# Optimization experiments

Measured on AMD Instinct MI355X. Metric: run time of the kernel, lower is better.

Reference implementation:

```python
import jax, jax.numpy as jnp
import numpy as np
from jax import lax

B, N, C = 16, 2304, 768
H_HEADS, D = 12, 64  # num_heads, head_dim
SCALE = 9.0 ** (-0.5)  # equivalent_head_dim ** -0.5


def setup_inputs() -> dict:
    key = jax.random.key(0)
    ks = jax.random.split(key, 8)
    return {
        "x": jax.random.normal(ks[0], (B, N, C), dtype=jnp.float32),
        "qkv_w": jax.random.normal(ks[1], (3 * C + 3 * D, C), dtype=jnp.float32) * 0.02,
        "qkv_b": jax.random.normal(ks[2], (3 * C + 3 * D,), dtype=jnp.float32) * 0.02,
        "w1": jax.random.normal(ks[3], (1, H_HEADS, D, D), dtype=jnp.float32) * 0.02,
        "w2": jax.random.normal(ks[4], (1, H_HEADS, D, D), dtype=jnp.float32) * 0.02,
        "w3": jax.random.normal(ks[5], (D, 1, 3, 3), dtype=jnp.float32) * 0.02,
        "proj_w": jax.random.normal(ks[6], (C, C + D), dtype=jnp.float32) * 0.02,
        "proj_b": jax.random.normal(ks[7], (C,), dtype=jnp.float32) * 0.02,
        "h": 48,
        "w": 48,
    }


def _inner_swiglu(k, v, w1, w2, lr=1.0):
    # k, v: [B, H, N, d]; w1, w2: [1, H, d, d]
    z1 = jnp.einsum('bhnd,hde->bhne', k, w1[0])
    z2 = jnp.einsum('bhnd,hde->bhne', k, w2[0])
    sig = jax.nn.sigmoid(z2)
    a = z2 * sig
    e = -v / float(v.shape[2]) * SCALE
    g1 = jnp.einsum('bhnd,bhne->bhde', k, e * a)
    g2 = jnp.einsum('bhnd,bhne->bhde', k, e * z1 * (sig * (1.0 + z2 * (1.0 - sig))))
    g1 = g1 / (jnp.linalg.norm(g1, axis=-2, keepdims=True) + 1.0)
    g2 = g2 / (jnp.linalg.norm(g2, axis=-2, keepdims=True) + 1.0)
    return w1 - lr * g1, w2 - lr * g2  # [B, H, d, d]


def _inner_3x3dwc(k, v, w3, hh, ww, lr=1.0):
    # k, v: [B, d, h, w]; w3: [d, 1, 3, 3]
    b, c = k.shape[0], k.shape[1]
    e = -v / float(hh * ww) * SCALE
    kp = jnp.pad(k, ((0, 0), (0, 0), (1, 1), (1, 1)))
    dots = []
    for ys in (0, 1, 2):  # 1 + dy
        for xs in (0, 1, 2):  # 1 + dx
            dots.append(jnp.sum(kp[:, :, ys:ys + hh, xs:xs + ww] * e, axis=(-2, -1)))
    g = jnp.stack(dots, axis=-1).reshape(b * c, 1, 3, 3)
    g = g / (jnp.sqrt(jnp.sum(g * g, axis=(-2, -1), keepdims=True)) + 1.0)
    return jnp.tile(w3, (b, 1, 1, 1)) - lr * g  # [B*d, 1, 3, 3]


def reference(x, qkv_w, qkv_b, w1, w2, w3, proj_w, proj_b, h, w):
    b, n, c = x.shape
    nh = w1.shape[1]
    d = c // nh
    qkv = x @ qkv_w.T + qkv_b  # [B, N, 3C + 3d]
    q1, k1, v1, q2, k2, v2 = jnp.split(
        qkv, [c, 2 * c, 3 * c, 3 * c + d, 3 * c + 2 * d], axis=-1)
    heads = lambda t: t.reshape(b, n, nh, d).transpose(0, 2, 1, 3)
    q1, k1, v1 = heads(q1), heads(k1), heads(v1)

    w1u, w2u = _inner_swiglu(k1, v1, w1, w2)
    x1 = jnp.einsum('bhnd,bhde->bhne', q1, w1u) * jax.nn.silu(
        jnp.einsum('bhnd,bhde->bhne', q1, w2u))
    x1 = x1.transpose(0, 2, 1, 3).reshape(b, n, c)

    spatial = lambda t: t.reshape(b, h, w, d).transpose(0, 3, 1, 2)  # [B, d, h, w]
    q2s, k2s, v2s = spatial(q2), spatial(k2), spatial(v2)
    w3u = _inner_3x3dwc(k2s, v2s, w3, h, w)
    x2 = lax.conv_general_dilated(
        q2s.reshape(1, b * d, h, w), w3u,
        window_strides=(1, 1), padding=((1, 1), (1, 1)),
        feature_group_count=b * d,
        dimension_numbers=('NCHW', 'OIHW', 'NCHW'))
    x2 = x2.reshape(b, d, n).transpose(0, 2, 1)  # [B, N, d]

    out = jnp.concatenate([x1, x2], axis=-1) @ proj_w.T + proj_b
    return out
```

## Files before the change

kernel.cpp:

```cpp
#include <hip/hip_runtime.h>
#include <hip/hip_bf16.h>
#include <math.h>

#define B_   16
#define N_   2304
#define C_   768
#define H_   12
#define D_   64
#define M_   (B_*N_)
#define NQKV 2496
#define NPAD 2560
#define CCP  896
#define EVS  (-1.0f/6912.0f)

typedef __bf16 bf16x8 __attribute__((ext_vector_type(8)));
typedef __bf16 bf16x4 __attribute__((ext_vector_type(4)));
typedef float  f32x4  __attribute__((ext_vector_type(4)));

static __device__ __forceinline__ void gload_lds16(const void* g, void* l) {
  __builtin_amdgcn_global_load_lds((const __attribute__((address_space(1))) void*)g,
                                   (__attribute__((address_space(3))) void*)l, 16, 0, 0);
}

static __device__ __forceinline__ bf16x8 ld8(const __bf16* p) {
  bf16x4 lo = *(const bf16x4*)p;
  bf16x4 hi = *(const bf16x4*)(p + 4);
  return __builtin_shufflevector(lo, hi, 0,1,2,3,4,5,6,7);
}

__global__ __launch_bounds__(256) void cvt_x(const float* __restrict__ in,
                                             __bf16* __restrict__ out, int n8) {
  int i = blockIdx.x * 256 + threadIdx.x;
  if (i >= n8) return;
  const float4* p = (const float4*)(in + (size_t)i * 8);
  float4 a = p[0], b = p[1];
  bf16x8 o = {(__bf16)a.x,(__bf16)a.y,(__bf16)a.z,(__bf16)a.w,
              (__bf16)b.x,(__bf16)b.y,(__bf16)b.z,(__bf16)b.w};
  *(bf16x8*)(out + (size_t)i * 8) = o;
}

__global__ __launch_bounds__(256) void cvt_wqkv(const float* __restrict__ w,
    const float* __restrict__ bias, __bf16* __restrict__ wout, float* __restrict__ bout) {
  int i = blockIdx.x * 256 + threadIdx.x;
  if (i < NPAD * 96) {
    int n = i / 96, c8 = i - n * 96;
    bf16x8 o;
    if (n < NQKV) {
      const float4* p = (const float4*)(w + (size_t)n * 768 + c8 * 8);
      float4 a = p[0], b = p[1];
      o = (bf16x8){(__bf16)a.x,(__bf16)a.y,(__bf16)a.z,(__bf16)a.w,
                   (__bf16)b.x,(__bf16)b.y,(__bf16)b.z,(__bf16)b.w};
    } else {
      o = (bf16x8){(__bf16)0.f,(__bf16)0.f,(__bf16)0.f,(__bf16)0.f,
                   (__bf16)0.f,(__bf16)0.f,(__bf16)0.f,(__bf16)0.f};
    }
    *(bf16x8*)(wout + (size_t)n * 768 + c8 * 8) = o;
  }
  if (i < NPAD) bout[i] = (i < NQKV) ? bias[i] : 0.0f;
}

__global__ __launch_bounds__(256) void cvt_pw(const float* __restrict__ in,
                                              __bf16* __restrict__ out) {
  int i = blockIdx.x * 256 + threadIdx.x;
  if (i >= 86016) return;
  int n = i / 112, c8 = i - n * 112;
  int k = c8 * 8;
  bf16x8 o;
  if (k < 832) {
    const float4* p = (const float4*)(in + (size_t)n * 832 + k);
    float4 a = p[0], b = p[1];
    o = (bf16x8){(__bf16)a.x,(__bf16)a.y,(__bf16)a.z,(__bf16)a.w,
                 (__bf16)b.x,(__bf16)b.y,(__bf16)b.z,(__bf16)b.w};
  } else {
    o = (bf16x8){(__bf16)0.f,(__bf16)0.f,(__bf16)0.f,(__bf16)0.f,
                 (__bf16)0.f,(__bf16)0.f,(__bf16)0.f,(__bf16)0.f};
  }
  *(bf16x8*)(out + (size_t)n * CCP + k) = o;
}

__global__ __launch_bounds__(256) void zeropad(__bf16* __restrict__ concat) {
  int i = blockIdx.x * 256 + threadIdx.x;
  if (i >= M_ * 8) return;
  int row = i >> 3, ch = i & 7;
  bf16x8 z = {(__bf16)0.f,(__bf16)0.f,(__bf16)0.f,(__bf16)0.f,
              (__bf16)0.f,(__bf16)0.f,(__bf16)0.f,(__bf16)0.f};
  *(bf16x8*)(concat + (size_t)row * CCP + 832 + ch * 8) = z;
}

template<int OUTF32>
__global__ __launch_bounds__(512, 2) void gemm8(
    const __bf16* __restrict__ A, const __bf16* __restrict__ Bt,
    const float* __restrict__ bias, void* __restrict__ Cout,
    const int K, const int ldc, const int nbn, const int KT)
{
  __shared__ __align__(16) __bf16 sA[2][2][128 * 64];
  __shared__ __align__(16) __bf16 sB[2][2][128 * 64];
  const int tid  = threadIdx.x;
  const int lane = tid & 63;
  const int wid  = tid >> 6;
  const int wm = wid >> 2;
  const int wn = wid & 3;
  const int l15 = lane & 15, lq = lane >> 4;

  const int nwg = gridDim.x;
  const int swz = ((int)blockIdx.x & 7) * (nwg >> 3) + ((int)blockIdx.x >> 3);
  const int bm = swz / nbn;
  const int bn = swz - bm * nbn;

  const int strow = tid >> 3;
  const int stoff = strow * 64 + (tid & 7) * 8;
  const __bf16* gA = A  + (size_t)((size_t)bm * 256 + strow) * K + ((tid & 7) ^ (strow & 7)) * 8;
  const __bf16* gB = Bt + (size_t)((size_t)bn * 256 + strow) * K + ((tid & 7) ^ (strow & 7)) * 8;

  f32x4 acc[2][4][2][2];
  #pragma unroll
  for (int a = 0; a < 2; ++a)
    #pragma unroll
    for (int m = 0; m < 4; ++m)
      #pragma unroll
      for (int b = 0; b < 2; ++b)
        #pragma unroll
        for (int n = 0; n < 2; ++n) acc[a][m][b][n] = (f32x4){0.f,0.f,0.f,0.f};

  bf16x8 af0[4][2], af1[4][2], bf0[2][2], bf1[2][2];

#define STAGE_A(q, h, T) do {                                                   \
    const size_t ko_ = (size_t)(T) * 64;                                        \
    gload_lds16(gA + (size_t)((h)*128 +  0) * K + ko_, &sA[q][h][stoff]);       \
    gload_lds16(gA + (size_t)((h)*128 + 64) * K + ko_, &sA[q][h][4096 + stoff]);\
  } while (0)
#define STAGE_B(q, h, T) do {                                                   \
    const size_t ko_ = (size_t)(T) * 64;                                        \
    gload_lds16(gB + (size_t)((h)*128 +  0) * K + ko_, &sB[q][h][stoff]);       \
    gload_lds16(gB + (size_t)((h)*128 + 64) * K + ko_, &sB[q][h][4096 + stoff]);\
  } while (0)
#define LOADA(DST, h, q) do {                                                   \
    _Pragma("unroll") for (int mf_ = 0; mf_ < 4; ++mf_) {                       \
      const int r_ = wm * 64 + mf_ * 16 + l15;                                  \
      _Pragma("unroll") for (int kk_ = 0; kk_ < 2; ++kk_)                       \
        DST[mf_][kk_] = *(const bf16x8*)&sA[q][h][r_ * 64 + (((kk_*4+lq) ^ (r_&7)) * 8)]; \
    } } while (0)
#define LOADB(DST, h, q) do {                                                   \
    _Pragma("unroll") for (int nf_ = 0; nf_ < 2; ++nf_) {                       \
      const int c_ = wn * 32 + nf_ * 16 + l15;                                  \
      _Pragma("unroll") for (int kk_ = 0; kk_ < 2; ++kk_)                       \
        DST[nf_][kk_] = *(const bf16x8*)&sB[q][h][c_ * 64 + (((kk_*4+lq) ^ (c_&7)) * 8)]; \
    } } while (0)
#define MMA(a_, b_, AF, BF) do {                                                \
    __builtin_amdgcn_s_setprio(1);                                              \
    _Pragma("unroll") for (int kk_ = 0; kk_ < 2; ++kk_)                         \
    _Pragma("unroll") for (int mf_ = 0; mf_ < 4; ++mf_)                         \
    _Pragma("unroll") for (int nf_ = 0; nf_ < 2; ++nf_)                         \
      acc[a_][mf_][b_][nf_] = __builtin_amdgcn_mfma_f32_16x16x32_bf16(          \
          AF[mf_][kk_], BF[nf_][kk_], acc[a_][mf_][b_][nf_], 0, 0, 0);          \
    __builtin_amdgcn_s_setprio(0);                                              \
  } while (0)
#define BAR  __builtin_amdgcn_s_barrier()
#define LGKM do { asm volatile("s_waitcnt lgkmcnt(0)" ::: "memory");            \
                  __builtin_amdgcn_sched_barrier(0); } while (0)
#define VMW4 asm volatile("s_waitcnt vmcnt(4)" ::: "memory")
#define VMW0 asm volatile("s_waitcnt vmcnt(0)" ::: "memory")

  STAGE_A(0, 0, 0); STAGE_A(0, 1, 0); STAGE_B(0, 0, 0); STAGE_B(0, 1, 0);
  STAGE_B(1, 0, 1);
  STAGE_A(1, 1, 1);
  VMW4;
  BAR;

  for (int t = 0; t < KT; t += 2) {
    LOADA(af0, 0, 0); LOADB(bf0, 0, 0);
    STAGE_A(1, 0, t + 1); STAGE_B(1, 1, t + 1);
    BAR; LGKM; MMA(0, 0, af0, bf0); BAR;
    LOADA(af1, 1, 0);
    BAR; LGKM; MMA(1, 0, af1, bf0); BAR;
    LOADB(bf1, 1, 0);
    if (t + 2 < KT) STAGE_B(0, 0, t + 2);
    BAR; LGKM; MMA(1, 1, af1, bf1); BAR;
    if (t + 2 < KT) STAGE_A(0, 1, t + 2);
    BAR; MMA(0, 1, af0, bf1);
    if (t + 2 < KT) { VMW4; } else { VMW0; }
    BAR;
    LOADA(af0, 0, 1); LOADB(bf0, 0, 1);
    if (t + 2 < KT) { STAGE_A(0, 0, t + 2); STAGE_B(0, 1, t + 2); }
    BAR; LGKM; MMA(0, 0, af0, bf0); BAR;
    LOADA(af1, 1, 1);
    BAR; LGKM; MMA(1, 0, af1, bf0); BAR;
    LOADB(bf1, 1, 1);
    if (t + 3 < KT) STAGE_B(1, 0, t + 3);
    BAR; LGKM; MMA(1, 1, af1, bf1); BAR;
    if (t + 3 < KT) STAGE_A(1, 1, t + 3);
    BAR; MMA(0, 1, af0, bf1);
    if (t + 3 < KT) { VMW4; } else { VMW0; }
    BAR;
  }
#undef STAGE_A
#undef STAGE_B
#undef LOADA
#undef LOADB
#undef MMA

  #pragma unroll
  for (int b = 0; b < 2; ++b)
    #pragma unroll
    for (int nf = 0; nf < 2; ++nf) {
      const int col = bn * 256 + b * 128 + wn * 32 + nf * 16 + l15;
      const float bs = bias[col];
      #pragma unroll
      for (int a = 0; a < 2; ++a)
        #pragma unroll
        for (int mf = 0; mf < 4; ++mf) {
          const int row0 = bm * 256 + a * 128 + wm * 64 + mf * 16 + lq * 4;
          #pragma unroll
          for (int r = 0; r < 4; ++r) {
            float v = acc[a][mf][b][nf][r] + bs;
            if (OUTF32) ((float*)Cout)[(size_t)(row0 + r) * ldc + col] = v;
            else        ((__bf16*)Cout)[(size_t)(row0 + r) * ldc + col] = (__bf16)v;
          }
        }
    }
}

__global__ __launch_bounds__(256, 3) void inner_grad(
    const __bf16* __restrict__ qkv, const float* __restrict__ w1,
    const float* __restrict__ w2, float* __restrict__ gpart)
{
  const int blk = blockIdx.x;
  const int bh = blk >> 2, seg = blk & 3;
  const int b = bh / H_, h = bh - b * H_;
  const int tid = threadIdx.x, wid = tid >> 6, lane = tid & 63;
  const int wr = wid >> 1, wc = wid & 1, l15 = lane & 15, lq = lane >> 4;

  __shared__ __bf16 w1T[64 * 72], w2T[64 * 72];
  __shared__ __bf16 kNt1[64 * 72];
  __shared__ __bf16 kT[64 * 72], t2T[64 * 72];

  const float* w1p = w1 + h * 4096;
  const float* w2p = w2 + h * 4096;
  for (int idx = tid; idx < 4096; idx += 256) {
    int d = idx >> 6, e = idx & 63;
    w1T[e * 72 + d] = (__bf16)w1p[idx];
    w2T[e * 72 + d] = (__bf16)w2p[idx];
  }

  f32x4 g1a[2][2], g2a[2][2];
  #pragma unroll
  for (int i = 0; i < 2; ++i)
    #pragma unroll
    for (int j = 0; j < 2; ++j) { g1a[i][j] = (f32x4){0.f,0.f,0.f,0.f}; g2a[i][j] = (f32x4){0.f,0.f,0.f,0.f}; }

  const size_t rowb = (size_t)b * N_;
  const int koff = C_ + h * D_;
  const int voff = 2 * C_ + h * D_;
  const int sn = tid >> 2, sdb = tid & 3;
  __syncthreads();

  for (int ci = 0; ci < 9; ++ci) {
    const int n0 = seg * 576 + ci * 64;
    {
      const __bf16* src = qkv + (rowb + n0 + sn) * (size_t)NPAD + koff + sdb * 16;
      bf16x8 va = *(const bf16x8*)src;
      bf16x8 vb = *(const bf16x8*)(src + 8);
      __bf16* kn = &kNt1[sn * 72 + sdb * 16];
      *(bf16x4*)(kn + 0)  = __builtin_shufflevector(va, va, 0,1,2,3);
      *(bf16x4*)(kn + 4)  = __builtin_shufflevector(va, va, 4,5,6,7);
      *(bf16x4*)(kn + 8)  = __builtin_shufflevector(vb, vb, 0,1,2,3);
      *(bf16x4*)(kn + 12) = __builtin_shufflevector(vb, vb, 4,5,6,7);
      #pragma unroll
      for (int j = 0; j < 8; ++j) kT[(sdb * 16 + j) * 72 + sn] = va[j];
      #pragma unroll
      for (int j = 0; j < 8; ++j) kT[(sdb * 16 + 8 + j) * 72 + sn] = vb[j];
    }
    __syncthreads();

    f32x4 z1[2][2], z2[2][2];
    #pragma unroll
    for (int i = 0; i < 2; ++i)
      #pragma unroll
      for (int j = 0; j < 2; ++j) { z1[i][j] = (f32x4){0.f,0.f,0.f,0.f}; z2[i][j] = (f32x4){0.f,0.f,0.f,0.f}; }
    #pragma unroll
    for (int kk = 0; kk < 2; ++kk) {
      bf16x8 af[2], b1[2], b2[2];
      #pragma unroll
      for (int mi = 0; mi < 2; ++mi)
        af[mi] = ld8(&kNt1[(wr * 32 + mi * 16 + l15) * 72 + kk * 32 + lq * 8]);
      #pragma unroll
      for (int ni = 0; ni < 2; ++ni) {
        int e = wc * 32 + ni * 16 + l15;
        b1[ni] = ld8(&w1T[e * 72 + kk * 32 + lq * 8]);
        b2[ni] = ld8(&w2T[e * 72 + kk * 32 + lq * 8]);
      }
      #pragma unroll
      for (int mi = 0; mi < 2; ++mi)
        #pragma unroll
        for (int ni = 0; ni < 2; ++ni) {
          z1[mi][ni] = __builtin_amdgcn_mfma_f32_16x16x32_bf16(af[mi], b1[ni], z1[mi][ni], 0, 0, 0);
          z2[mi][ni] = __builtin_amdgcn_mfma_f32_16x16x32_bf16(af[mi], b2[ni], z2[mi][ni], 0, 0, 0);
        }
    }
    __syncthreads();

    #pragma unroll
    for (int mi = 0; mi < 2; ++mi)
      #pragma unroll
      for (int ni = 0; ni < 2; ++ni) {
        int nl = wr * 32 + mi * 16 + lq * 4;
        int e  = wc * 32 + ni * 16 + l15;
        const __bf16* vp = qkv + (rowb + n0 + nl) * (size_t)NPAD + voff + e;
        #pragma unroll
        for (int r = 0; r < 4; ++r) {
          float vv  = (float)vp[(size_t)r * NPAD];
          float ev  = vv * EVS;
          float z1v = z1[mi][ni][r], z2v = z2[mi][ni][r];
          float sg  = 1.0f / (1.0f + __expf(-z2v));
          float t1  = ev * (z2v * sg);
          float t2  = ev * z1v * (sg * (1.0f + z2v * (1.0f - sg)));
          kNt1[e * 72 + nl + r] = (__bf16)t1;
          t2T [e * 72 + nl + r] = (__bf16)t2;
        }
      }
    __syncthreads();

    #pragma unroll
    for (int kk = 0; kk < 2; ++kk) {
      bf16x8 af[2], b1[2], b2[2];
      #pragma unroll
      for (int mi = 0; mi < 2; ++mi)
        af[mi] = ld8(&kT[(wr * 32 + mi * 16 + l15) * 72 + kk * 32 + lq * 8]);
      #pragma unroll
      for (int ni = 0; ni < 2; ++ni) {
        int e = wc * 32 + ni * 16 + l15;
        b1[ni] = ld8(&kNt1[e * 72 + kk * 32 + lq * 8]);
        b2[ni] = ld8(&t2T [e * 72 + kk * 32 + lq * 8]);
      }
      #pragma unroll
      for (int mi = 0; mi < 2; ++mi)
        #pragma unroll
        for (int ni = 0; ni < 2; ++ni) {
          g1a[mi][ni] = __builtin_amdgcn_mfma_f32_16x16x32_bf16(af[mi], b1[ni], g1a[mi][ni], 0, 0, 0);
          g2a[mi][ni] = __builtin_amdgcn_mfma_f32_16x16x32_bf16(af[mi], b2[ni], g2a[mi][ni], 0, 0, 0);
        }
    }
    __syncthreads();
  }

  float* gp = gpart + (size_t)blk * 8192;
  #pragma unroll
  for (int mi = 0; mi < 2; ++mi)
    #pragma unroll
    for (int ni = 0; ni < 2; ++ni)
      #pragma unroll
      for (int r = 0; r < 4; ++r) {
        int d = wr * 32 + mi * 16 + lq * 4 + r;
        int e = wc * 32 + ni * 16 + l15;
        gp[d * 64 + e]        = g1a[mi][ni][r];
        gp[4096 + d * 64 + e] = g2a[mi][ni][r];
      }
}

__global__ __launch_bounds__(256) void inner_upd(
    const float* __restrict__ gpart, const float* __restrict__ w1,
    const float* __restrict__ w2, __bf16* __restrict__ wu)
{
  const int bh = blockIdx.x;
  const int h = bh % H_;
  const int tid = threadIdx.x;
  __shared__ float g1[64 * 65], g2[64 * 65];
  __shared__ float nrm1[64], nrm2[64];
  const float* w1p = w1 + h * 4096;
  const float* w2p = w2 + h * 4096;

  for (int idx = tid; idx < 4096; idx += 256) {
    float s1 = 0.f, s2 = 0.f;
    #pragma unroll
    for (int s = 0; s < 4; ++s) {
      const float* gp = gpart + (size_t)(bh * 4 + s) * 8192;
      s1 += gp[idx]; s2 += gp[4096 + idx];
    }
    int d = idx >> 6, e = idx & 63;
    g1[d * 65 + e] = s1; g2[d * 65 + e] = s2;
  }
  __syncthreads();
  if (tid < 128) {
    const float* gs = (tid < 64) ? g1 : g2;
    int e = tid & 63;
    float s = 0.f;
    for (int d = 0; d < 64; ++d) { float gv = gs[d * 65 + e]; s += gv * gv; }
    float rn = 1.0f / (sqrtf(s) + 1.0f);
    if (tid < 64) nrm1[e] = rn; else nrm2[e] = rn;
  }
  __syncthreads();
  __bf16* wub = wu + (size_t)bh * 8192;
  for (int idx = tid; idx < 4096; idx += 256) {
    int d = idx >> 6, e = idx & 63;
    wub[idx]        = (__bf16)(w1p[idx] - g1[d * 65 + e] * nrm1[e]);
    wub[4096 + idx] = (__bf16)(w2p[idx] - g2[d * 65 + e] * nrm2[e]);
  }
}

__global__ __launch_bounds__(256) void inner_apply(
    const __bf16* __restrict__ qkv, const __bf16* __restrict__ wu,
    __bf16* __restrict__ concat)
{
  const int blk = blockIdx.x;
  const int bh = blk / 6, seg = blk - bh * 6;
  const int b = bh / H_, h = bh - b * H_;
  const int tid = threadIdx.x, wid = tid >> 6, lane = tid & 63;
  const int wr = wid >> 1, wc = wid & 1, l15 = lane & 15, lq = lane >> 4;

  __shared__ __bf16 w1T[64 * 72], w2T[64 * 72], qN[64 * 72];
  const __bf16* wub = wu + (size_t)bh * 8192;
  for (int idx = tid; idx < 4096; idx += 256) {
    int d = idx >> 6, e = idx & 63;
    w1T[e * 72 + d] = wub[idx];
    w2T[e * 72 + d] = wub[4096 + idx];
  }

  const size_t rowb = (size_t)b * N_;
  const int qoff = h * D_;
  const int sn = tid >> 2, sdb = tid & 3;

  for (int ci = 0; ci < 6; ++ci) {
    const int n0 = seg * 384 + ci * 64;
    {
      const __bf16* src = qkv + (rowb + n0 + sn) * (size_t)NPAD + qoff + sdb * 16;
      bf16x8 va = *(const bf16x8*)src;
      bf16x8 vb = *(const bf16x8*)(src + 8);
      __bf16* kn = &qN[sn * 72 + sdb * 16];
      *(bf16x4*)(kn + 0)  = __builtin_shufflevector(va, va, 0,1,2,3);
      *(bf16x4*)(kn + 4)  = __builtin_shufflevector(va, va, 4,5,6,7);
      *(bf16x4*)(kn + 8)  = __builtin_shufflevector(vb, vb, 0,1,2,3);
      *(bf16x4*)(kn + 12) = __builtin_shufflevector(vb, vb, 4,5,6,7);
    }
    __syncthreads();
    f32x4 y1[2][2], y2[2][2];
    #pragma unroll
    for (int i = 0; i < 2; ++i)
      #pragma unroll
      for (int j = 0; j < 2; ++j) { y1[i][j] = (f32x4){0.f,0.f,0.f,0.f}; y2[i][j] = (f32x4){0.f,0.f,0.f,0.f}; }
    #pragma unroll
    for (int kk = 0; kk < 2; ++kk) {
      bf16x8 af[2], b1[2], b2[2];
      #pragma unroll
      for (int mi = 0; mi < 2; ++mi)
        af[mi] = ld8(&qN[(wr * 32 + mi * 16 + l15) * 72 + kk * 32 + lq * 8]);
      #pragma unroll
      for (int ni = 0; ni < 2; ++ni) {
        int e = wc * 32 + ni * 16 + l15;
        b1[ni] = ld8(&w1T[e * 72 + kk * 32 + lq * 8]);
        b2[ni] = ld8(&w2T[e * 72 + kk * 32 + lq * 8]);
      }
      #pragma unroll
      for (int mi = 0; mi < 2; ++mi)
        #pragma unroll
        for (int ni = 0; ni < 2; ++ni) {
          y1[mi][ni] = __builtin_amdgcn_mfma_f32_16x16x32_bf16(af[mi], b1[ni], y1[mi][ni], 0, 0, 0);
          y2[mi][ni] = __builtin_amdgcn_mfma_f32_16x16x32_bf16(af[mi], b2[ni], y2[mi][ni], 0, 0, 0);
        }
    }
    #pragma unroll
    for (int mi = 0; mi < 2; ++mi)
      #pragma unroll
      for (int ni = 0; ni < 2; ++ni) {
        int nl = wr * 32 + mi * 16 + lq * 4;
        int e  = wc * 32 + ni * 16 + l15;
        #pragma unroll
        for (int r = 0; r < 4; ++r) {
          float a1 = y1[mi][ni][r], a2 = y2[mi][ni][r];
          float sg = 1.0f / (1.0f + __expf(-a2));
          concat[(rowb + n0 + nl + r) * (size_t)CCP + h * D_ + e] = (__bf16)(a1 * (a2 * sg));
        }
      }
    __syncthreads();
  }
}

__global__ __launch_bounds__(256) void dwc_grad2(const __bf16* __restrict__ qkv,
                                                 float* __restrict__ w3p) {
  const int blk = blockIdx.x;
  const int b = blk / 12, sp = blk - b * 12;
  const int tid = threadIdx.x, dd = tid & 63, rl = tid >> 6;
  __shared__ __bf16 kS[6 * 50 * 64];
  __shared__ float red[4][9][64];
  for (int i = tid; i < 9600; i += 256) ((unsigned*)kS)[i] = 0u;
  __syncthreads();
  const size_t base = (size_t)b * N_ * NPAD;
  for (int i = tid; i < 6 * 48 * 8; i += 256) {
    int y6 = i / 384; int rem = i - y6 * 384; int x = rem >> 3; int c8 = rem & 7;
    int y = 4 * sp - 1 + y6;
    if (y >= 0 && y < 48) {
      int p = y * 48 + x;
      bf16x8 v = *(const bf16x8*)&qkv[base + (size_t)p * NPAD + 2368 + c8 * 8];
      *(bf16x8*)&kS[((y6 * 50) + x + 1) * 64 + c8 * 8] = v;
    }
  }
  __syncthreads();
  float acc[9];
  #pragma unroll
  for (int j = 0; j < 9; ++j) acc[j] = 0.f;
  const int y = 4 * sp + rl;
  for (int x = 0; x < 48; ++x) {
    int p = y * 48 + x;
    float e = (float)qkv[base + (size_t)p * NPAD + 2432 + dd] * EVS;
    #pragma unroll
    for (int j = 0; j < 9; ++j) {
      int ys = j / 3, xs = j - ys * 3;
      acc[j] += (float)kS[((rl + ys) * 50 + x + xs) * 64 + dd] * e;
    }
  }
  #pragma unroll
  for (int j = 0; j < 9; ++j) red[rl][j][dd] = acc[j];
  __syncthreads();
  if (rl == 0) {
    #pragma unroll
    for (int j = 0; j < 9; ++j) {
      float s = red[0][j][dd] + red[1][j][dd] + red[2][j][dd] + red[3][j][dd];
      w3p[((size_t)(b * 12 + sp) * 64 + dd) * 9 + j] = s;
    }
  }
}

__global__ __launch_bounds__(256) void dwc_upd(const float* __restrict__ w3p,
    const float* __restrict__ w3, float* __restrict__ w3u) {
  int i = blockIdx.x * 256 + threadIdx.x;
  if (i >= 1024) return;
  int b = i >> 6, dd = i & 63;
  float g[9];
  #pragma unroll
  for (int j = 0; j < 9; ++j) g[j] = 0.f;
  for (int sp = 0; sp < 12; ++sp)
    #pragma unroll
    for (int j = 0; j < 9; ++j)
      g[j] += w3p[((size_t)(b * 12 + sp) * 64 + dd) * 9 + j];
  float ss = 0.f;
  #pragma unroll
  for (int j = 0; j < 9; ++j) ss += g[j] * g[j];
  float rn = 1.0f / (sqrtf(ss) + 1.0f);
  #pragma unroll
  for (int j = 0; j < 9; ++j) w3u[i * 9 + j] = w3[dd * 9 + j] - g[j] * rn;
}

__global__ __launch_bounds__(256) void dwc_apply2(const __bf16* __restrict__ qkv,
    const float* __restrict__ w3u, __bf16* __restrict__ concat) {
  const int blk = blockIdx.x;
  const int b = blk / 12, sp = blk - b * 12;
  const int tid = threadIdx.x, dd = tid & 63, rl = tid >> 6;
  __shared__ __bf16 qS[6 * 50 * 64];
  for (int i = tid; i < 9600; i += 256) ((unsigned*)qS)[i] = 0u;
  __syncthreads();
  const size_t base = (size_t)b * N_ * NPAD;
  for (int i = tid; i < 6 * 48 * 8; i += 256) {
    int y6 = i / 384; int rem = i - y6 * 384; int x = rem >> 3; int c8 = rem & 7;
    int y = 4 * sp - 1 + y6;
    if (y >= 0 && y < 48) {
      int p = y * 48 + x;
      bf16x8 v = *(const bf16x8*)&qkv[base + (size_t)p * NPAD + 2304 + c8 * 8];
      *(bf16x8*)&qS[((y6 * 50) + x + 1) * 64 + c8 * 8] = v;
    }
  }
  __syncthreads();
  float wv[9];
  #pragma unroll
  for (int j = 0; j < 9; ++j) wv[j] = w3u[(size_t)(b * 64 + dd) * 9 + j];
  const int y = 4 * sp + rl;
  for (int x = 0; x < 48; ++x) {
    float s = 0.f;
    #pragma unroll
    for (int j = 0; j < 9; ++j) {
      int ys = j / 3, xs = j - ys * 3;
      s += (float)qS[((rl + ys) * 50 + x + xs) * 64 + dd] * wv[j];
    }
    int p = y * 48 + x;
    concat[((size_t)b * N_ + p) * CCP + 768 + dd] = (__bf16)s;
  }
}

extern "C" void kernel_launch(void* const* d_in, const int* in_sizes, int n_in,
                              void* d_out, int out_size, void* d_ws, size_t ws_size,
                              hipStream_t stream) {
  const float* x      = (const float*)d_in[0];
  const float* qkv_w  = (const float*)d_in[1];
  const float* qkv_b  = (const float*)d_in[2];
  const float* w1     = (const float*)d_in[3];
  const float* w2     = (const float*)d_in[4];
  const float* w3     = (const float*)d_in[5];
  const float* proj_w = (const float*)d_in[6];
  const float* proj_b = (const float*)d_in[7];

  char* ws = (char*)d_ws;
  __bf16* xb     = (__bf16*)ws;
  __bf16* wqkvb  = (__bf16*)(ws + 56623104);
  float*  qkvbp  = (float*) (ws + 60555264);
  __bf16* concat = (__bf16*)ws;
  __bf16* qkvb16 = (__bf16*)(ws + 66060288);
  __bf16* pwb    = (__bf16*)(ws + 254803968);
  float*  w3u    = (float*) (ws + 256180224);
  float*  w3p    = (float*) (ws + 256217088);
  float*  gpart  = (float*) (ws + 256659456);
  __bf16* wu     = (__bf16*)(ws + 281825280);

  cvt_x   <<<13824, 256, 0, stream>>>(x, xb, 3538944);
  cvt_wqkv<<<  960, 256, 0, stream>>>(qkv_w, qkv_b, wqkvb, qkvbp);
  cvt_pw  <<<  336, 256, 0, stream>>>(proj_w, pwb);

  gemm8<0><<<1440, 512, 0, stream>>>(xb, wqkvb, qkvbp, (void*)qkvb16,
                                     768, NPAD, 10, 12);

  zeropad<<<1152, 256, 0, stream>>>(concat);
  inner_grad <<< 768, 256, 0, stream>>>(qkvb16, w1, w2, gpart);
  inner_upd  <<< 192, 256, 0, stream>>>(gpart, w1, w2, wu);
  inner_apply<<<1152, 256, 0, stream>>>(qkvb16, wu, concat);
  dwc_grad2 <<<192, 256, 0, stream>>>(qkvb16, w3p);
  dwc_upd   <<<  4, 256, 0, stream>>>(w3p, w3, w3u);
  dwc_apply2<<<192, 256, 0, stream>>>(qkvb16, w3u, concat);

  gemm8<1><<<432, 512, 0, stream>>>(concat, pwb, proj_b, d_out,
                                    CCP, 768, 3, 14);
}
```

Baseline: 442.9 us.

## Switch GEMM to 32x32x16 MFMA, fuse conversions, drop K padding

The GEMM inner loop now issues 32x32x16 bf16 MFMAs with 16-wide accumulators instead of 16x16x32, which reduces LDS fragment reads per FLOP and changes the register layout of the epilogue. The three fp32-to-bf16 conversion kernels are merged into one launch. The concat/proj K dimension is no longer padded from 832 to 896, which removes the zeropad kernel and one K-tile of the final GEMM. An odd-KT tail path is added to handle the resulting 13 tiles. Risks are higher register pressure from the larger accumulators and a tail path that runs without pipelining.

```diff
diff --git a/kernel.cpp b/kernel.cpp
--- a/kernel.cpp
+++ b/kernel.cpp
@@ -10,12 +10,13 @@
 #define M_   (B_*N_)
 #define NQKV 2496
 #define NPAD 2560
-#define CCP  896
+#define CCP  832
 #define EVS  (-1.0f/6912.0f)
 
 typedef __bf16 bf16x8 __attribute__((ext_vector_type(8)));
 typedef __bf16 bf16x4 __attribute__((ext_vector_type(4)));
 typedef float  f32x4  __attribute__((ext_vector_type(4)));
+typedef float  f32x16 __attribute__((ext_vector_type(16)));
 
 static __device__ __forceinline__ void gload_lds16(const void* g, void* l) {
   __builtin_amdgcn_global_load_lds((const __attribute__((address_space(1))) void*)g,
@@ -28,25 +29,26 @@
   return __builtin_shufflevector(lo, hi, 0,1,2,3,4,5,6,7);
 }
 
-__global__ __launch_bounds__(256) void cvt_x(const float* __restrict__ in,
-                                             __bf16* __restrict__ out, int n8) {
-  int i = blockIdx.x * 256 + threadIdx.x;
-  if (i >= n8) return;
-  const float4* p = (const float4*)(in + (size_t)i * 8);
-  float4 a = p[0], b = p[1];
-  bf16x8 o = {(__bf16)a.x,(__bf16)a.y,(__bf16)a.z,(__bf16)a.w,
-              (__bf16)b.x,(__bf16)b.y,(__bf16)b.z,(__bf16)b.w};
-  *(bf16x8*)(out + (size_t)i * 8) = o;
-}
-
-__global__ __launch_bounds__(256) void cvt_wqkv(const float* __restrict__ w,
-    const float* __restrict__ bias, __bf16* __restrict__ wout, float* __restrict__ bout) {
-  int i = blockIdx.x * 256 + threadIdx.x;
-  if (i < NPAD * 96) {
+__global__ __launch_bounds__(256) void cvt_all(
+    const float* __restrict__ x, const float* __restrict__ qkv_w,
+    const float* __restrict__ qkv_b, const float* __restrict__ proj_w,
+    __bf16* __restrict__ xb, __bf16* __restrict__ wqkvb,
+    float* __restrict__ qkvbp, __bf16* __restrict__ pwb)
+{
+  const int blk = blockIdx.x;
+  if (blk < 13824) {
+    int i = blk * 256 + threadIdx.x;
+    const float4* p = (const float4*)(x + (size_t)i * 8);
+    float4 a = p[0], b = p[1];
+    bf16x8 o = {(__bf16)a.x,(__bf16)a.y,(__bf16)a.z,(__bf16)a.w,
+                (__bf16)b.x,(__bf16)b.y,(__bf16)b.z,(__bf16)b.w};
+    *(bf16x8*)(xb + (size_t)i * 8) = o;
+  } else if (blk < 14784) {
+    int i = (blk - 13824) * 256 + threadIdx.x;
     int n = i / 96, c8 = i - n * 96;
     bf16x8 o;
     if (n < NQKV) {
-      const float4* p = (const float4*)(w + (size_t)n * 768 + c8 * 8);
+      const float4* p = (const float4*)(qkv_w + (size_t)n * 768 + c8 * 8);
       float4 a = p[0], b = p[1];
       o = (bf16x8){(__bf16)a.x,(__bf16)a.y,(__bf16)a.z,(__bf16)a.w,
                    (__bf16)b.x,(__bf16)b.y,(__bf16)b.z,(__bf16)b.w};
@@ -54,37 +56,17 @@
       o = (bf16x8){(__bf16)0.f,(__bf16)0.f,(__bf16)0.f,(__bf16)0.f,
                    (__bf16)0.f,(__bf16)0.f,(__bf16)0.f,(__bf16)0.f};
     }
-    *(bf16x8*)(wout + (size_t)n * 768 + c8 * 8) = o;
-  }
-  if (i < NPAD) bout[i] = (i < NQKV) ? bias[i] : 0.0f;
-}
-
-__global__ __launch_bounds__(256) void cvt_pw(const float* __restrict__ in,
-                                              __bf16* __restrict__ out) {
-  int i = blockIdx.x * 256 + threadIdx.x;
-  if (i >= 86016) return;
-  int n = i / 112, c8 = i - n * 112;
-  int k = c8 * 8;
-  bf16x8 o;
-  if (k < 832) {
-    const float4* p = (const float4*)(in + (size_t)n * 832 + k);
+    *(bf16x8*)(wqkvb + (size_t)n * 768 + c8 * 8) = o;
+    if (i < NPAD) qkvbp[i] = (i < NQKV) ? qkv_b[i] : 0.0f;
+  } else {
+    int i = (blk - 14784) * 256 + threadIdx.x;
+    if (i >= 79872) return;
+    const float4* p = (const float4*)(proj_w + (size_t)i * 8);
     float4 a = p[0], b = p[1];
-    o = (bf16x8){(__bf16)a.x,(__bf16)a.y,(__bf16)a.z,(__bf16)a.w,
-                 (__bf16)b.x,(__bf16)b.y,(__bf16)b.z,(__bf16)b.w};
-  } else {
-    o = (bf16x8){(__bf16)0.f,(__bf16)0.f,(__bf16)0.f,(__bf16)0.f,
-                 (__bf16)0.f,(__bf16)0.f,(__bf16)0.f,(__bf16)0.f};
-  }
-  *(bf16x8*)(out + (size_t)n * CCP + k) = o;
-}
-
-__global__ __launch_bounds__(256) void zeropad(__bf16* __restrict__ concat) {
-  int i = blockIdx.x * 256 + threadIdx.x;
-  if (i >= M_ * 8) return;
-  int row = i >> 3, ch = i & 7;
-  bf16x8 z = {(__bf16)0.f,(__bf16)0.f,(__bf16)0.f,(__bf16)0.f,
-              (__bf16)0.f,(__bf16)0.f,(__bf16)0.f,(__bf16)0.f};
-  *(bf16x8*)(concat + (size_t)row * CCP + 832 + ch * 8) = z;
+    bf16x8 o = {(__bf16)a.x,(__bf16)a.y,(__bf16)a.z,(__bf16)a.w,
+                (__bf16)b.x,(__bf16)b.y,(__bf16)b.z,(__bf16)b.w};
+    *(bf16x8*)(pwb + (size_t)i * 8) = o;
+  }
 }
 
 template<int OUTF32>
@@ -100,7 +82,7 @@
   const int wid  = tid >> 6;
   const int wm = wid >> 2;
   const int wn = wid & 3;
-  const int l15 = lane & 15, lq = lane >> 4;
+  const int l31 = lane & 31, lh = lane >> 5;
 
   const int nwg = gridDim.x;
   const int swz = ((int)blockIdx.x & 7) * (nwg >> 3) + ((int)blockIdx.x >> 3);
@@ -112,17 +94,17 @@
   const __bf16* gA = A  + (size_t)((size_t)bm * 256 + strow) * K + ((tid & 7) ^ (strow & 7)) * 8;
   const __bf16* gB = Bt + (size_t)((size_t)bn * 256 + strow) * K + ((tid & 7) ^ (strow & 7)) * 8;
 
-  f32x4 acc[2][4][2][2];
+  f32x16 acc[2][2][2];
   #pragma unroll
   for (int a = 0; a < 2; ++a)
     #pragma unroll
-    for (int m = 0; m < 4; ++m)
+    for (int mt = 0; mt < 2; ++mt)
       #pragma unroll
       for (int b = 0; b < 2; ++b)
         #pragma unroll
-        for (int n = 0; n < 2; ++n) acc[a][m][b][n] = (f32x4){0.f,0.f,0.f,0.f};
-
-  bf16x8 af0[4][2], af1[4][2], bf0[2][2], bf1[2][2];
+        for (int z = 0; z < 16; ++z) acc[a][mt][b][z] = 0.f;
+
+  bf16x8 af0[2][4], af1[2][4], bf0[4], bf1[4];
 
 #define STAGE_A(q, h, T) do {                                                   \
     const size_t ko_ = (size_t)(T) * 64;                                        \
@@ -135,24 +117,22 @@
     gload_lds16(gB + (size_t)((h)*128 + 64) * K + ko_, &sB[q][h][4096 + stoff]);\
   } while (0)
 #define LOADA(DST, h, q) do {                                                   \
-    _Pragma("unroll") for (int mf_ = 0; mf_ < 4; ++mf_) {                       \
-      const int r_ = wm * 64 + mf_ * 16 + l15;                                  \
-      _Pragma("unroll") for (int kk_ = 0; kk_ < 2; ++kk_)                       \
-        DST[mf_][kk_] = *(const bf16x8*)&sA[q][h][r_ * 64 + (((kk_*4+lq) ^ (r_&7)) * 8)]; \
+    _Pragma("unroll") for (int mt_ = 0; mt_ < 2; ++mt_) {                       \
+      const int r_ = wm * 64 + mt_ * 32 + l31;                                  \
+      _Pragma("unroll") for (int s_ = 0; s_ < 4; ++s_)                          \
+        DST[mt_][s_] = *(const bf16x8*)&sA[q][h][r_ * 64 + (((s_*2+lh) ^ (r_&7)) * 8)]; \
     } } while (0)
 #define LOADB(DST, h, q) do {                                                   \
-    _Pragma("unroll") for (int nf_ = 0; nf_ < 2; ++nf_) {                       \
-      const int c_ = wn * 32 + nf_ * 16 + l15;                                  \
-      _Pragma("unroll") for (int kk_ = 0; kk_ < 2; ++kk_)                       \
-        DST[nf_][kk_] = *(const bf16x8*)&sB[q][h][c_ * 64 + (((kk_*4+lq) ^ (c_&7)) * 8)]; \
-    } } while (0)
+    const int c_ = wn * 32 + l31;                                               \
+    _Pragma("unroll") for (int s_ = 0; s_ < 4; ++s_)                            \
+      DST[s_] = *(const bf16x8*)&sB[q][h][c_ * 64 + (((s_*2+lh) ^ (c_&7)) * 8)]; \
+  } while (0)
 #define MMA(a_, b_, AF, BF) do {                                                \
     __builtin_amdgcn_s_setprio(1);                                              \
-    _Pragma("unroll") for (int kk_ = 0; kk_ < 2; ++kk_)                         \
-    _Pragma("unroll") for (int mf_ = 0; mf_ < 4; ++mf_)                         \
-    _Pragma("unroll") for (int nf_ = 0; nf_ < 2; ++nf_)                         \
-      acc[a_][mf_][b_][nf_] = __builtin_amdgcn_mfma_f32_16x16x32_bf16(          \
-          AF[mf_][kk_], BF[nf_][kk_], acc[a_][mf_][b_][nf_], 0, 0, 0);          \
+    _Pragma("unroll") for (int s_ = 0; s_ < 4; ++s_)                            \
+    _Pragma("unroll") for (int mt_ = 0; mt_ < 2; ++mt_)                         \
+      acc[a_][mt_][b_] = __builtin_amdgcn_mfma_f32_32x32x16_bf16(               \
+          AF[mt_][s_], BF[s_], acc[a_][mt_][b_], 0, 0, 0);                      \
     __builtin_amdgcn_s_setprio(0);                                              \
   } while (0)
 #define BAR  __builtin_amdgcn_s_barrier()
@@ -167,7 +147,7 @@
   VMW4;
   BAR;
 
-  for (int t = 0; t < KT; t += 2) {
+  for (int t = 0; t + 1 < KT; t += 2) {
     LOADA(af0, 0, 0); LOADB(bf0, 0, 0);
     STAGE_A(1, 0, t + 1); STAGE_B(1, 1, t + 1);
     BAR; LGKM; MMA(0, 0, af0, bf0); BAR;
@@ -193,6 +173,15 @@
     if (t + 3 < KT) { VMW4; } else { VMW0; }
     BAR;
   }
+  if (KT & 1) {
+    LOADA(af0, 0, 0); LOADB(bf0, 0, 0);
+    MMA(0, 0, af0, bf0);
+    LOADA(af1, 1, 0);
+    MMA(1, 0, af1, bf0);
+    LOADB(bf1, 1, 0);
+    MMA(1, 1, af1, bf1);
+    MMA(0, 1, af0, bf1);
+  }
 #undef STAGE_A
 #undef STAGE_B
 #undef LOADA
@@ -200,24 +189,25 @@
 #undef MMA
 
   #pragma unroll
-  for (int b = 0; b < 2; ++b)
-    #pragma unroll
-    for (int nf = 0; nf < 2; ++nf) {
-      const int col = bn * 256 + b * 128 + wn * 32 + nf * 16 + l15;
-      const float bs = bias[col];
-      #pragma unroll
-      for (int a = 0; a < 2; ++a)
+  for (int b = 0; b < 2; ++b) {
+    const int col = bn * 256 + b * 128 + wn * 32 + l31;
+    const float bs = bias[col];
+    #pragma unroll
+    for (int a = 0; a < 2; ++a)
+      #pragma unroll
+      for (int mt = 0; mt < 2; ++mt) {
+        const int row0 = bm * 256 + a * 128 + wm * 64 + mt * 32 + 4 * lh;
         #pragma unroll
-        for (int mf = 0; mf < 4; ++mf) {
-          const int row0 = bm * 256 + a * 128 + wm * 64 + mf * 16 + lq * 4;
+        for (int g = 0; g < 4; ++g)
           #pragma unroll
           for (int r = 0; r < 4; ++r) {
-            float v = acc[a][mf][b][nf][r] + bs;
-            if (OUTF32) ((float*)Cout)[(size_t)(row0 + r) * ldc + col] = v;
-            else        ((__bf16*)Cout)[(size_t)(row0 + r) * ldc + col] = (__bf16)v;
+            const int row = row0 + g * 8 + r;
+            float v = acc[a][mt][b][g * 4 + r] + bs;
+            if (OUTF32) ((float*)Cout)[(size_t)row * ldc + col] = v;
+            else        ((__bf16*)Cout)[(size_t)row * ldc + col] = (__bf16)v;
           }
-        }
-    }
+      }
+  }
 }
 
 __global__ __launch_bounds__(256, 3) void inner_grad(
@@ -598,14 +588,11 @@
   float*  gpart  = (float*) (ws + 256659456);
   __bf16* wu     = (__bf16*)(ws + 281825280);
 
-  cvt_x   <<<13824, 256, 0, stream>>>(x, xb, 3538944);
-  cvt_wqkv<<<  960, 256, 0, stream>>>(qkv_w, qkv_b, wqkvb, qkvbp);
-  cvt_pw  <<<  336, 256, 0, stream>>>(proj_w, pwb);
+  cvt_all<<<15096, 256, 0, stream>>>(x, qkv_w, qkv_b, proj_w, xb, wqkvb, qkvbp, pwb);
 
   gemm8<0><<<1440, 512, 0, stream>>>(xb, wqkvb, qkvbp, (void*)qkvb16,
                                      768, NPAD, 10, 12);
 
-  zeropad<<<1152, 256, 0, stream>>>(concat);
   inner_grad <<< 768, 256, 0, stream>>>(qkvb16, w1, w2, gpart);
   inner_upd  <<< 192, 256, 0, stream>>>(gpart, w1, w2, wu);
   inner_apply<<<1152, 256, 0, stream>>>(qkvb16, wu, concat);
@@ -614,5 +601,5 @@
   dwc_apply2<<<192, 256, 0, stream>>>(qkvb16, w3u, concat);
 
   gemm8<1><<<432, 512, 0, stream>>>(concat, pwb, proj_b, d_out,
-                                    CCP, 768, 3, 14);
-}
+                                    832, 768, 3, 13);
+}
```

New measurement: 497.0 us. 1.12x slower.
